# Optimization experiments

Measured on AMD Instinct MI355X. Metric: run time of the kernel, lower is better.

The kernel has to match this reference:

```python
import math
import jax, jax.numpy as jnp
import numpy as np

S = 64.0
M = 0.5
C = 1.5
K = 16
EPS = 1e-6
IN = 128
OUT = 10000
B = 1024


def _l2norm(x, axis):
    # matches torch.nn.functional.normalize (eps=1e-12)
    n = jnp.linalg.norm(x, axis=axis, keepdims=True)
    return x / jnp.maximum(n, 1e-12)


def setup_inputs() -> dict:
    key = jax.random.key(0)
    k1, k2, k3, k4 = jax.random.split(key, 4)
    inp = jax.random.normal(k1, (B, IN), dtype=jnp.float32)
    factor = jax.random.uniform(k2, (B, 1), dtype=jnp.float32)
    label = jax.random.randint(k3, (B,), 0, OUT)
    # xavier_uniform over (k, in, out): fan_in=IN, fan_out=OUT (last two dims)
    limit = math.sqrt(6.0 / (IN + OUT))
    weight = jax.random.uniform(k4, (K, IN, OUT), dtype=jnp.float32, minval=-limit, maxval=limit)
    return {"input": inp, "factor": factor, "label": label, "weight": weight}


def reference(input, factor, label, weight):
    # disguise-adaptive margin: (B,1)
    func_a = jnp.power(C, factor / 12.0) * M
    threshold = math.pi - func_a  # (B,1)

    xn = _l2norm(input, axis=1)          # (B, IN)
    wn = _l2norm(weight, axis=1)         # (K, IN, OUT), normalized along IN

    # batched sub-center matmul then max over sub-centers k
    cos_all = jnp.einsum('bf,kfo->kbo', xn, wn)   # (K, B, OUT)
    cos_theta = jnp.max(cos_all, axis=0)          # (B, OUT)

    theta = jnp.arccos(jnp.clip(cos_theta, -1.0 + EPS, 1.0 - EPS))
    one_hot = jax.nn.one_hot(label, OUT, dtype=theta.dtype)  # (B, OUT)
    selected = jnp.where(theta > threshold, jnp.zeros_like(one_hot), one_hot)
    logits = jnp.cos(jnp.where(selected.astype(bool), theta + func_a, theta)) * S

    # cross-entropy (mean reduction)
    logp = jax.nn.log_softmax(logits, axis=-1)
    cls_loss = -jnp.mean(jnp.take_along_axis(logp, label[:, None], axis=1))

    # top-1 accuracy (percent), detached stat
    pred = jnp.argmax(logits, axis=1)
    prec1 = jnp.mean((pred == label).astype(jnp.float32)) * 100.0
    return cls_loss, prec1
```

## Files before the change

kernel.cpp:

```cpp
#include <hip/hip_runtime.h>
#include <hip/hip_bf16.h>
#include <math.h>

#define BB    1024
#define FIN   128
#define NOUT  10000
#define NBLK  79
#define NCB   158
#define NK    16
#define NPART (NCB * 2)
#define LDX   136

typedef __attribute__((ext_vector_type(8))) short short8;
typedef __attribute__((ext_vector_type(4))) float floatx4;

__device__ __forceinline__ unsigned packbf(float a, float b) {
    __hip_bfloat162 h = __float22bfloat162_rn(make_float2(a, b));
    union { __hip_bfloat162 h2; unsigned u; } v;
    v.h2 = h;
    return v.u;
}

__device__ __forceinline__ unsigned scale2(unsigned p, float wi) {
    float lo = __uint_as_float(p << 16) * wi;
    float hi = __uint_as_float(p & 0xffff0000u) * wi;
    return packbf(lo, hi);
}

__device__ __forceinline__ void async16(const void* g, void* l) {
    __builtin_amdgcn_global_load_lds(
        (const __attribute__((address_space(1))) unsigned int*)g,
        (__attribute__((address_space(3))) unsigned int*)l, 16, 0, 0);
}

__global__ void rowprep(const float* __restrict__ X, const float* __restrict__ factor,
                        float* __restrict__ xinv, float* __restrict__ fa_out,
                        float* __restrict__ thr_out) {
    int b = blockIdx.x;
    int lane = threadIdx.x;
    float v0 = X[b * FIN + lane];
    float v1 = X[b * FIN + 64 + lane];
    float s = v0 * v0 + v1 * v1;
    #pragma unroll
    for (int off = 32; off > 0; off >>= 1) s += __shfl_down(s, off);
    if (lane == 0) {
        xinv[b] = 1.0f / fmaxf(sqrtf(s), 1e-12f);
        float fa = powf(1.5f, factor[b] * (1.0f / 12.0f)) * 0.5f;
        fa_out[b] = fa;
        thr_out[b] = (float)M_PI - fa;
    }
}

__global__ __launch_bounds__(256) void wconv(
    const float* __restrict__ W, unsigned char* __restrict__ Wbf,
    const float* __restrict__ X, const float* __restrict__ factor,
    float* __restrict__ xinv, float* __restrict__ fa_out, float* __restrict__ thr_out) {

    __shared__ float sqp[16][64];
    __shared__ float wis[64];

    const int tid = threadIdx.x;

    if (blockIdx.x >= NK * NCB) {
        int rb = blockIdx.x - NK * NCB;
        int w4 = tid >> 6, lane = tid & 63;
        for (int i = w4; i < 64; i += 4) {
            int row = rb * 64 + i;
            float v0 = X[row * FIN + lane];
            float v1 = X[row * FIN + 64 + lane];
            float ss = v0 * v0 + v1 * v1;
            #pragma unroll
            for (int off = 32; off > 0; off >>= 1) ss += __shfl_down(ss, off);
            if (lane == 0) {
                xinv[row] = 1.0f / fmaxf(sqrtf(ss), 1e-12f);
                float fa = powf(1.5f, factor[row] * (1.0f / 12.0f)) * 0.5f;
                fa_out[row] = fa;
                thr_out[row] = (float)M_PI - fa;
            }
        }
        return;
    }

    const int k  = blockIdx.x / NCB;
    const int cb = blockIdx.x - k * NCB;
    const int o0 = cb * 64;

    const int fb = tid >> 4;
    const int c4 = tid & 15;
    const int o  = o0 + c4 * 4;
    const bool ov = o < NOUT;

    float4 v[8];
    const float* Wp = W + (size_t)(k * FIN + fb * 8) * NOUT + o;
    #pragma unroll
    for (int j = 0; j < 8; j++)
        v[j] = ov ? *(const float4*)(Wp + (size_t)j * NOUT)
                  : make_float4(0.f, 0.f, 0.f, 0.f);

    float s0 = 0.f, s1 = 0.f, s2 = 0.f, s3 = 0.f;
    #pragma unroll
    for (int j = 0; j < 8; j++) {
        s0 = fmaf(v[j].x, v[j].x, s0);
        s1 = fmaf(v[j].y, v[j].y, s1);
        s2 = fmaf(v[j].z, v[j].z, s2);
        s3 = fmaf(v[j].w, v[j].w, s3);
    }
    *(float4*)(&sqp[fb][c4 * 4]) = make_float4(s0, s1, s2, s3);
    __syncthreads();

    if (tid < 64) {
        float t = 0.f;
        #pragma unroll
        for (int f2 = 0; f2 < 16; f2++) t += sqp[f2][tid];
        wis[tid] = 1.0f / fmaxf(sqrtf(t), 1e-12f);
    }
    __syncthreads();

    const int kk = fb >> 2, q = fb & 3;
    unsigned char* dst = Wbf + ((size_t)k * NCB + cb) * 16384;
    #pragma unroll
    for (int i = 0; i < 4; i++) {
        int col = c4 * 4 + i;
        int wn = col >> 5, n2 = (col >> 4) & 1, l15 = col & 15;
        float wi = wis[col];
        uint4 u;
        u.x = scale2(packbf((&v[0].x)[i], (&v[1].x)[i]), wi);
        u.y = scale2(packbf((&v[2].x)[i], (&v[3].x)[i]), wi);
        u.z = scale2(packbf((&v[4].x)[i], (&v[5].x)[i]), wi);
        u.w = scale2(packbf((&v[6].x)[i], (&v[7].x)[i]), wi);
        *(uint4*)(dst + wn * 8192 + n2 * 4096 + kk * 1024 + q * 256 + l15 * 16) = u;
    }
}

__global__ __launch_bounds__(512, 2) void gemm_mx(
    const float* __restrict__ X, const unsigned char* __restrict__ Wbf,
    const int* __restrict__ label, const float* __restrict__ xinv,
    float2* __restrict__ partial, float* __restrict__ cosl) {

    __shared__ union {
        short xs[128 * LDX];
        short bb[2][16384];
    } u;

    const int tid  = threadIdx.x;
    const int lane = tid & 63;
    const int w    = tid >> 6;
    const int l15  = lane & 15;
    const int q    = lane >> 4;
    const int wm   = w & 3;
    const int wn   = w >> 2;

    const int id    = blockIdx.x;
    const int group = id >> 6;
    const int sub   = id & 63;
    const int cb    = group * 8 + (sub & 7);
    const int y     = sub >> 3;
    if (cb >= NCB) return;
    const int r0 = y * 128;
    const int o0 = cb * 64;

    #pragma unroll
    for (int it = 0; it < 8; it++) {
        int idx = it * 512 + tid;
        int row = idx >> 5;
        int c4  = idx & 31;
        const float4 v = *(const float4*)(X + (size_t)(r0 + row) * FIN + c4 * 4);
        float xi = xinv[r0 + row];
        uint2 p;
        p.x = packbf(v.x * xi, v.y * xi);
        p.y = packbf(v.z * xi, v.w * xi);
        *(uint2*)(u.xs + row * LDX + c4 * 4) = p;
    }
    __syncthreads();

    short8 af[2][4];
    #pragma unroll
    for (int mt = 0; mt < 2; mt++)
        #pragma unroll
        for (int kk = 0; kk < 4; kk++)
            af[mt][kk] = *(const short8*)(u.xs + (wm * 32 + mt * 16 + l15) * LDX + kk * 32 + q * 8);
    __syncthreads();

    auto issue2 = [&](int s, short* d) {
        const unsigned char* g = Wbf + ((size_t)(2 * s) * NCB + cb) * 16384
                                 + (size_t)w * 2048 + (size_t)lane * 16;
        short* dw = d + w * 1024;
        async16(g, dw);
        async16(g + 1024, dw + 512);
        const unsigned char* g2 = g + (size_t)NCB * 16384;
        short* dw2 = d + 8192 + w * 1024;
        async16(g2, dw2);
        async16(g2 + 1024, dw2 + 512);
    };

    short* cur = u.bb[0];
    short* nxt = u.bb[1];

    issue2(0, cur);

    floatx4 maxv[2][2];
    #pragma unroll
    for (int mt = 0; mt < 2; mt++)
        #pragma unroll
        for (int n2 = 0; n2 < 2; n2++)
            #pragma unroll
            for (int r = 0; r < 4; r++)
                maxv[mt][n2][r] = -INFINITY;

    for (int s = 0; s < NK / 2; s++) {
        asm volatile("s_waitcnt vmcnt(0)" ::: "memory");
        __builtin_amdgcn_s_barrier();
        if (s < NK / 2 - 1) issue2(s + 1, nxt);

        #pragma unroll
        for (int half = 0; half < 2; half++) {
            const short* wt = cur + half * 8192;

            floatx4 acc[2][2];
            #pragma unroll
            for (int mt = 0; mt < 2; mt++)
                #pragma unroll
                for (int n2 = 0; n2 < 2; n2++)
                    acc[mt][n2] = (floatx4){0.f, 0.f, 0.f, 0.f};
            #pragma unroll
            for (int kk = 0; kk < 4; kk++) {
                short8 bf[2];
                #pragma unroll
                for (int n2 = 0; n2 < 2; n2++)
                    bf[n2] = *(const short8*)(wt + wn * 4096 + n2 * 2048 + kk * 512 + lane * 8);
                #pragma unroll
                for (int mt = 0; mt < 2; mt++)
                    #pragma unroll
                    for (int n2 = 0; n2 < 2; n2++)
                        acc[mt][n2] = __builtin_amdgcn_mfma_f32_16x16x32_bf16(
                            af[mt][kk], bf[n2], acc[mt][n2], 0, 0, 0);
            }
            #pragma unroll
            for (int mt = 0; mt < 2; mt++)
                #pragma unroll
                for (int n2 = 0; n2 < 2; n2++)
                    #pragma unroll
                    for (int r = 0; r < 4; r++)
                        maxv[mt][n2][r] = fmaxf(maxv[mt][n2][r], acc[mt][n2][r]);
        }

        short* t = cur; cur = nxt; nxt = t;
    }

    #pragma unroll
    for (int mt = 0; mt < 2; mt++) {
        #pragma unroll
        for (int rr = 0; rr < 4; rr++) {
            int row = r0 + wm * 32 + mt * 16 + q * 4 + rr;
            int lb = label[row];
            float m = -1e30f, sum = 0.f;
            #pragma unroll
            for (int n2 = 0; n2 < 2; n2++) {
                int o = o0 + wn * 32 + n2 * 16 + l15;
                if (o < NOUT) {
                    float cc = maxv[mt][n2][rr];
                    if (o == lb) {
                        cosl[row] = cc;
                    } else {
                        float l = 64.0f * fminf(fmaxf(cc, -1.0f + 1e-6f), 1.0f - 1e-6f);
                        sum += __expf(l - 64.0f);
                        m = fmaxf(m, l);
                    }
                }
            }
            #pragma unroll
            for (int off = 1; off <= 8; off <<= 1) {
                sum += __shfl_xor(sum, off);
                m = fmaxf(m, __shfl_xor(m, off));
            }
            if (l15 == 0)
                partial[(size_t)row * NPART + cb * 2 + wn] = make_float2(m, sum);
        }
    }
}

__global__ __launch_bounds__(256, 2) void gemm_stats(
    const float* __restrict__ X, const float* __restrict__ W,
    const int* __restrict__ label, const float* __restrict__ xinv,
    float2* __restrict__ partial, float* __restrict__ cosl) {

    __shared__ short xs[128 * LDX];
    __shared__ short wt[128 * LDX];
    __shared__ float sqs[128][2];

    const int tid  = threadIdx.x;
    const int lane = tid & 63;
    const int w    = tid >> 6;
    const int l15  = lane & 15;
    const int q    = lane >> 4;
    const int wm   = w & 1;
    const int wn   = w >> 1;

    const int id    = blockIdx.x;
    const int group = id >> 6;
    const int sub   = id & 63;
    const int jb    = group * 8 + (sub & 7);
    const int y     = sub >> 3;
    if (jb >= NBLK) return;
    const int r0 = y * 128;
    const int o0 = jb * 128;

    #pragma unroll
    for (int it = 0; it < 16; it++) {
        int idx = it * 256 + tid;
        int row = idx >> 5;
        int c4  = idx & 31;
        const float4 v = *(const float4*)(X + (size_t)(r0 + row) * FIN + c4 * 4);
        uint2 p;
        p.x = packbf(v.x, v.y);
        p.y = packbf(v.z, v.w);
        *(uint2*)(xs + row * LDX + c4 * 4) = p;
    }

    const int st_o = (w & 1) * 64 + lane;
    const int st_f = (w >> 1) * 64;
    const int st_h = w >> 1;
    const int go   = o0 + st_o;
    const bool ov  = go < NOUT;

    float rw[64];
    {
        const float* Wp = W + (size_t)st_f * NOUT + go;
        #pragma unroll
        for (int g = 0; g < 16; g++)
            #pragma unroll
            for (int cc = 0; cc < 4; cc++)
                rw[g * 4 + cc] = ov ? Wp[(size_t)(g * 4 + cc) * NOUT] : 0.0f;
    }
    __syncthreads();

    short8 af[4][4];
    #pragma unroll
    for (int mt = 0; mt < 4; mt++)
        #pragma unroll
        for (int kk = 0; kk < 4; kk++)
            af[mt][kk] = *(const short8*)(xs + (wm * 64 + mt * 16 + l15) * LDX + kk * 32 + q * 8);

    floatx4 maxv[4][4];
    #pragma unroll
    for (int mt = 0; mt < 4; mt++)
        #pragma unroll
        for (int nt = 0; nt < 4; nt++)
            #pragma unroll
            for (int r = 0; r < 4; r++)
                maxv[mt][nt][r] = -INFINITY;

    for (int k = 0; k < NK; k++) {
        float sq = 0.0f;
        uint2 pk[16];
        #pragma unroll
        for (int g = 0; g < 16; g++) {
            float a0 = rw[g * 4 + 0], a1 = rw[g * 4 + 1];
            float a2 = rw[g * 4 + 2], a3 = rw[g * 4 + 3];
            sq = fmaf(a0, a0, sq); sq = fmaf(a1, a1, sq);
            sq = fmaf(a2, a2, sq); sq = fmaf(a3, a3, sq);
            pk[g].x = packbf(a0, a1);
            pk[g].y = packbf(a2, a3);
        }
        __syncthreads();
        #pragma unroll
        for (int g = 0; g < 16; g++)
            *(uint2*)(wt + st_o * LDX + st_f + g * 4) = pk[g];
        sqs[st_o][st_h] = sq;
        __syncthreads();

        if (k < NK - 1) {
            const float* Wn = W + ((size_t)(k + 1) * FIN + st_f) * NOUT + go;
            #pragma unroll
            for (int g = 0; g < 16; g++)
                #pragma unroll
                for (int cc = 0; cc < 4; cc++)
                    rw[g * 4 + cc] = ov ? Wn[(size_t)(g * 4 + cc) * NOUT] : 0.0f;
        }

        float wv[4];
        #pragma unroll
        for (int nt = 0; nt < 4; nt++) {
            int colx = wn * 64 + nt * 16 + l15;
            wv[nt] = 1.0f / fmaxf(sqrtf(sqs[colx][0] + sqs[colx][1]), 1e-12f);
        }

        #pragma unroll
        for (int h = 0; h < 2; h++) {
            floatx4 acc[4][2];
            #pragma unroll
            for (int mt = 0; mt < 4; mt++) {
                acc[mt][0] = (floatx4){0.f, 0.f, 0.f, 0.f};
                acc[mt][1] = (floatx4){0.f, 0.f, 0.f, 0.f};
            }
            #pragma unroll
            for (int kk = 0; kk < 4; kk++) {
                short8 bf0 = *(const short8*)(wt + (wn * 64 + (h * 2 + 0) * 16 + l15) * LDX + kk * 32 + q * 8);
                short8 bf1 = *(const short8*)(wt + (wn * 64 + (h * 2 + 1) * 16 + l15) * LDX + kk * 32 + q * 8);
                #pragma unroll
                for (int mt = 0; mt < 4; mt++) {
                    acc[mt][0] = __builtin_amdgcn_mfma_f32_16x16x32_bf16(af[mt][kk], bf0, acc[mt][0], 0, 0, 0);
                    acc[mt][1] = __builtin_amdgcn_mfma_f32_16x16x32_bf16(af[mt][kk], bf1, acc[mt][1], 0, 0, 0);
                }
            }
            #pragma unroll
            for (int mt = 0; mt < 4; mt++)
                #pragma unroll
                for (int n2 = 0; n2 < 2; n2++)
                    #pragma unroll
                    for (int r = 0; r < 4; r++)
                        maxv[mt][h * 2 + n2][r] =
                            fmaxf(maxv[mt][h * 2 + n2][r], acc[mt][n2][r] * wv[h * 2 + n2]);
        }
    }

    #pragma unroll
    for (int mt = 0; mt < 4; mt++) {
        #pragma unroll
        for (int rr = 0; rr < 4; rr++) {
            int row = r0 + wm * 64 + mt * 16 + q * 4 + rr;
            float xi = xinv[row];
            int lb = label[row];
            float m = -1e30f, sum = 0.f;
            #pragma unroll
            for (int nt = 0; nt < 4; nt++) {
                int o = o0 + wn * 64 + nt * 16 + l15;
                if (o < NOUT) {
                    float cc = maxv[mt][nt][rr] * xi;
                    if (o == lb) {
                        cosl[row] = cc;
                    } else {
                        float l = 64.0f * fminf(fmaxf(cc, -1.0f + 1e-6f), 1.0f - 1e-6f);
                        sum += __expf(l - 64.0f);
                        m = fmaxf(m, l);
                    }
                }
            }
            #pragma unroll
            for (int off = 1; off <= 8; off <<= 1) {
                sum += __shfl_xor(sum, off);
                m = fmaxf(m, __shfl_xor(m, off));
            }
            if (l15 == 0) {
                partial[(size_t)row * NPART + jb * 4 + wn * 2 + 0] = make_float2(m, sum);
                partial[(size_t)row * NPART + jb * 4 + wn * 2 + 1] = make_float2(-1e30f, 0.f);
            }
        }
    }
}

__global__ void finalize_rows(const float2* __restrict__ partial, const float* __restrict__ cosl,
                              const float* __restrict__ fa, const float* __restrict__ thr,
                              float2* __restrict__ rowres, int np) {
    int w = threadIdx.x >> 6;
    int lane = threadIdx.x & 63;
    int b = blockIdx.x * 4 + w;
    float m = -1e30f, s = 0.0f;
    for (int j = lane; j < np; j += 64) {
        float2 p = partial[(size_t)b * np + j];
        s += p.y;
        m = fmaxf(m, p.x);
    }
    #pragma unroll
    for (int off = 1; off < 64; off <<= 1) {
        s += __shfl_xor(s, off);
        m = fmaxf(m, __shfl_xor(m, off));
    }
    if (lane == 0) {
        float c = fminf(fmaxf(cosl[b], -1.0f + 1e-6f), 1.0f - 1e-6f);
        float theta = acosf(c);
        float ll = (theta > thr[b]) ? 64.0f * c : 64.0f * cosf(theta + fa[b]);
        float S = s + __expf(ll - 64.0f);
        float loss = 64.0f + logf(S) - ll;
        rowres[b] = make_float2(loss, (ll > m) ? 100.0f : 0.0f);
    }
}

__global__ void finalize_sum(const float2* __restrict__ rowres, float* __restrict__ out) {
    __shared__ float sl[1024];
    __shared__ float sc[1024];
    int b = threadIdx.x;
    float2 v = rowres[b];
    sl[b] = v.x;
    sc[b] = v.y;
    __syncthreads();
    for (int st = 512; st > 0; st >>= 1) {
        if (b < st) { sl[b] += sl[b + st]; sc[b] += sc[b + st]; }
        __syncthreads();
    }
    if (b == 0) {
        out[0] = sl[0] * (1.0f / 1024.0f);
        out[1] = sc[0] * (1.0f / 1024.0f);
    }
}

extern "C" void kernel_launch(void* const* d_in, const int* in_sizes, int n_in,
                              void* d_out, int out_size, void* d_ws, size_t ws_size,
                              hipStream_t stream) {
    const float* X      = (const float*)d_in[0];
    const float* factor = (const float*)d_in[1];
    const int*   label  = (const int*)d_in[2];
    const float* W      = (const float*)d_in[3];
    float* out = (float*)d_out;
    float* ws  = (float*)d_ws;

    float*  xinv = ws;
    float*  fa   = ws + 1024;
    float*  thr  = ws + 2048;
    float*  cosl = ws + 3072;
    float2* rowres = (float2*)(ws + 4096);
    float2* partial = (float2*)(ws + 6144);
    unsigned char* Wbf = (unsigned char*)d_ws + 4 * 1024 * 1024;

    const size_t wbf_bytes = (size_t)NK * NCB * 16384;
    const size_t need = 4ull * 1024 * 1024 + wbf_bytes;

    if (ws_size >= need) {
        wconv<<<NK * NCB + 16, 256, 0, stream>>>(W, Wbf, X, factor, xinv, fa, thr);
        gemm_mx<<<1280, 512, 0, stream>>>(X, Wbf, label, xinv, partial, cosl);
    } else {
        rowprep<<<BB, 64, 0, stream>>>(X, factor, xinv, fa, thr);
        gemm_stats<<<640, 256, 0, stream>>>(X, W, label, xinv, partial, cosl);
    }
    finalize_rows<<<BB / 4, 256, 0, stream>>>(partial, cosl, fa, thr, rowres, NPART);
    finalize_sum<<<1, BB, 0, stream>>>(rowres, out);
}
```

Before: 205.7 us.

## Restructure weight conversion to wider column tiles staged through LDS

The weight normalize-and-convert kernel now processes 256 output columns per block instead of 64. Each block streams all 128 input rows with full-row-width coalesced float4 loads, stores bf16 values in a shared-memory tile, and then transposes and scales them into the packed MFMA layout. The goal is more coalesced global reads and fewer blocks (640 instead of 2528). The cost is 64KB of LDS per block, which limits occupancy, plus an extra pass through shared memory.

```diff
diff --git a/kernel.cpp b/kernel.cpp
--- a/kernel.cpp
+++ b/kernel.cpp
@@ -10,6 +10,8 @@
 #define NK    16
 #define NPART (NCB * 2)
 #define LDX   136
+#define NCG   40
+#define OMAX  (NCB * 64)
 
 typedef __attribute__((ext_vector_type(8))) short short8;
 typedef __attribute__((ext_vector_type(4))) float floatx4;
@@ -56,13 +58,14 @@
     const float* __restrict__ X, const float* __restrict__ factor,
     float* __restrict__ xinv, float* __restrict__ fa_out, float* __restrict__ thr_out) {
 
-    __shared__ float sqp[16][64];
-    __shared__ float wis[64];
+    __shared__ unsigned short st[128][256];
+    __shared__ float4 sqp[4][64];
+    __shared__ float wis[256];
 
     const int tid = threadIdx.x;
 
-    if (blockIdx.x >= NK * NCB) {
-        int rb = blockIdx.x - NK * NCB;
+    if (blockIdx.x >= NK * NCG) {
+        int rb = blockIdx.x - NK * NCG;
         int w4 = tid >> 6, lane = tid & 63;
         for (int i = w4; i < 64; i += 4) {
             int row = rb * 64 + i;
@@ -81,54 +84,78 @@
         return;
     }
 
-    const int k  = blockIdx.x / NCB;
-    const int cb = blockIdx.x - k * NCB;
-    const int o0 = cb * 64;
-
-    const int fb = tid >> 4;
-    const int c4 = tid & 15;
-    const int o  = o0 + c4 * 4;
-    const bool ov = o < NOUT;
-
-    float4 v[8];
-    const float* Wp = W + (size_t)(k * FIN + fb * 8) * NOUT + o;
-    #pragma unroll
-    for (int j = 0; j < 8; j++)
-        v[j] = ov ? *(const float4*)(Wp + (size_t)j * NOUT)
-                  : make_float4(0.f, 0.f, 0.f, 0.f);
+    const int k  = blockIdx.x / NCG;
+    const int cg = blockIdx.x - k * NCG;
+    const int o0 = cg * 256;
+
+    const int fl = tid >> 6;
+    const int c4 = tid & 63;
+    const int oc = o0 + c4 * 4;
+    const bool ok = oc < NOUT;
 
     float s0 = 0.f, s1 = 0.f, s2 = 0.f, s3 = 0.f;
-    #pragma unroll
-    for (int j = 0; j < 8; j++) {
-        s0 = fmaf(v[j].x, v[j].x, s0);
-        s1 = fmaf(v[j].y, v[j].y, s1);
-        s2 = fmaf(v[j].z, v[j].z, s2);
-        s3 = fmaf(v[j].w, v[j].w, s3);
-    }
-    *(float4*)(&sqp[fb][c4 * 4]) = make_float4(s0, s1, s2, s3);
+    const float* Wp = W + (size_t)(k * FIN) * NOUT + oc;
+    #pragma unroll 8
+    for (int stp = 0; stp < 32; stp++) {
+        int f = stp * 4 + fl;
+        float4 v = ok ? *(const float4*)(Wp + (size_t)f * NOUT)
+                      : make_float4(0.f, 0.f, 0.f, 0.f);
+        s0 = fmaf(v.x, v.x, s0);
+        s1 = fmaf(v.y, v.y, s1);
+        s2 = fmaf(v.z, v.z, s2);
+        s3 = fmaf(v.w, v.w, s3);
+        uint2 p;
+        p.x = packbf(v.x, v.y);
+        p.y = packbf(v.z, v.w);
+        *(uint2*)&st[f][c4 * 4] = p;
+    }
+    sqp[fl][c4] = make_float4(s0, s1, s2, s3);
     __syncthreads();
 
-    if (tid < 64) {
-        float t = 0.f;
-        #pragma unroll
-        for (int f2 = 0; f2 < 16; f2++) t += sqp[f2][tid];
+    {
+        const float* sp = (const float*)sqp;
+        float t = sp[tid] + sp[256 + tid] + sp[512 + tid] + sp[768 + tid];
         wis[tid] = 1.0f / fmaxf(sqrtf(t), 1e-12f);
     }
     __syncthreads();
 
-    const int kk = fb >> 2, q = fb & 3;
-    unsigned char* dst = Wbf + ((size_t)k * NCB + cb) * 16384;
-    #pragma unroll
-    for (int i = 0; i < 4; i++) {
-        int col = c4 * 4 + i;
-        int wn = col >> 5, n2 = (col >> 4) & 1, l15 = col & 15;
-        float wi = wis[col];
-        uint4 u;
-        u.x = scale2(packbf((&v[0].x)[i], (&v[1].x)[i]), wi);
-        u.y = scale2(packbf((&v[2].x)[i], (&v[3].x)[i]), wi);
-        u.z = scale2(packbf((&v[4].x)[i], (&v[5].x)[i]), wi);
-        u.w = scale2(packbf((&v[6].x)[i], (&v[7].x)[i]), wi);
-        *(uint4*)(dst + wn * 8192 + n2 * 4096 + kk * 1024 + q * 256 + l15 * 16) = u;
+    const int hp = tid >> 7;
+    const int cp = tid & 127;
+    const int ce = cp * 2;
+    const int oe = o0 + ce;
+    if (oe < OMAX) {
+        const float wie = wis[ce];
+        const float wio = wis[ce + 1];
+        const int cb = oe >> 6;
+        const int c5 = oe & 63;
+        unsigned char* dst = Wbf + ((size_t)k * NCB + cb) * 16384
+                             + (c5 >> 5) * 8192 + ((c5 >> 4) & 1) * 4096
+                             + (c5 & 15) * 16;
+        #pragma unroll
+        for (int fbL = 0; fbL < 8; fbL++) {
+            int fb = hp * 8 + fbL;
+            int f0 = fb * 8;
+            unsigned a0 = *(const unsigned*)&st[f0 + 0][ce];
+            unsigned b0 = *(const unsigned*)&st[f0 + 1][ce];
+            unsigned a1 = *(const unsigned*)&st[f0 + 2][ce];
+            unsigned b1 = *(const unsigned*)&st[f0 + 3][ce];
+            unsigned a2 = *(const unsigned*)&st[f0 + 4][ce];
+            unsigned b2 = *(const unsigned*)&st[f0 + 5][ce];
+            unsigned a3 = *(const unsigned*)&st[f0 + 6][ce];
+            unsigned b3 = *(const unsigned*)&st[f0 + 7][ce];
+            uint4 ue, uo;
+            ue.x = scale2((a0 & 0xffffu) | (b0 << 16), wie);
+            uo.x = scale2((a0 >> 16) | (b0 & 0xffff0000u), wio);
+            ue.y = scale2((a1 & 0xffffu) | (b1 << 16), wie);
+            uo.y = scale2((a1 >> 16) | (b1 & 0xffff0000u), wio);
+            ue.z = scale2((a2 & 0xffffu) | (b2 << 16), wie);
+            uo.z = scale2((a2 >> 16) | (b2 & 0xffff0000u), wio);
+            ue.w = scale2((a3 & 0xffffu) | (b3 << 16), wie);
+            uo.w = scale2((a3 >> 16) | (b3 & 0xffff0000u), wio);
+            unsigned char* d = dst + (fb >> 2) * 1024 + (fb & 3) * 256;
+            *(uint4*)(d) = ue;
+            *(uint4*)(d + 16) = uo;
+        }
     }
 }
 
@@ -516,7 +543,7 @@
     const size_t need = 4ull * 1024 * 1024 + wbf_bytes;
 
     if (ws_size >= need) {
-        wconv<<<NK * NCB + 16, 256, 0, stream>>>(W, Wbf, X, factor, xinv, fa, thr);
+        wconv<<<NK * NCG + 16, 256, 0, stream>>>(W, Wbf, X, factor, xinv, fa, thr);
         gemm_mx<<<1280, 512, 0, stream>>>(X, Wbf, label, xinv, partial, cosl);
     } else {
         rowprep<<<BB, 64, 0, stream>>>(X, factor, xinv, fa, thr);
```

Result: no change. 207.0 us (+0.6%).
